# Kernel optimization log

Measured on AMD Instinct MI355X. Metric: run time of the kernel, lower is better.

The kernel has to match this reference:

```python
import jax, jax.numpy as jnp
import numpy as np

B, L, SEQ_D, PAIR_D = 4, 512, 640, 128
C, H, NL = 128, 4, 3
DH = C // H
ED = PAIR_D + 1
KNN_K = 16
E_MAX = 131072
MIN_LOOP, MIN_PROB, HP_THRESH = 4, 0.01, 0.3


def _nussinov_pairs_np(P, min_loop=MIN_LOOP, min_prob=MIN_PROB):
    # Faithful numpy port of the torch.jit Nussinov DP (vectorized over diagonals)
    Ln = P.shape[0]
    S = np.zeros((Ln, Ln), dtype=np.float64)
    lo = np.where(P >= min_prob, np.log(P / (1.0 - P + 1e-9)), 0.0)
    for d in range(min_loop + 1, Ln):
        i = np.arange(Ln - d); j = i + d
        cand = np.maximum(np.maximum(S[i + 1, j], S[i, j - 1]), S[i + 1, j - 1] + lo[i, j])
        cand = np.maximum(cand, 0.0)  # best_bif starts at 0
        if d - min_loop - 1 > 0:
            K = np.arange(1, d - min_loop)
            bif = (S[i[:, None], i[:, None] + K[None, :]] + S[i[:, None] + K[None, :] + 1, j[:, None]]).max(1)
            cand = np.maximum(cand, bif)
        S[i, j] = cand
    pairs = []; stack = [(0, Ln - 1)]; tol = 1e-9
    while stack:
        i, j = stack.pop()
        if i >= j:
            continue
        if abs(S[i, j] - S[i + 1, j]) <= tol:
            stack.append((i + 1, j))
        elif abs(S[i, j] - S[i, j - 1]) <= tol:
            stack.append((i, j - 1))
        elif P[i, j] >= min_prob and abs(S[i, j] - (S[i + 1, j - 1] + lo[i, j])) <= tol:
            pairs.append((i, j)); stack.append((i + 1, j - 1))
        else:
            for k in range(i + 1, j):
                if abs(S[i, j] - (S[i, k] + S[k + 1, j])) <= tol:
                    stack.append((i, k)); stack.append((k + 1, j)); break
    return pairs


def _build_edges_np(coords, bppm):
    # backbone + Nussinov secondary-structure + kNN + high-prob BPPM edges (per sample)
    Ln = coords.shape[0]
    a = np.arange(Ln - 1)
    src = [np.concatenate([a, a + 1])]; dst = [np.concatenate([a + 1, a])]
    ss = _nussinov_pairs_np(bppm)
    pair_set = set((min(s, d), max(s, d)) for s, d in ss)
    if ss:
        s_ = np.array([p[0] for p in ss]); d_ = np.array([p[1] for p in ss])
        src.append(np.concatenate([s_, d_])); dst.append(np.concatenate([d_, s_]))
    dist = np.linalg.norm(coords[:, None, :] - coords[None, :, :], axis=-1)
    np.fill_diagonal(dist, np.inf)
    nn = np.argpartition(dist, KNN_K, axis=1)[:, :KNN_K]
    s_k = np.repeat(np.arange(Ln), KNN_K); d_k = nn.reshape(-1)
    src.append(np.concatenate([s_k, d_k])); dst.append(np.concatenate([d_k, s_k]))
    hp = np.triu(bppm >= HP_THRESH, 1)
    idx = np.arange(Ln - 1); hp[idx, idx + 1] = False
    for (pi, pj) in pair_set:
        hp[pi, pj] = False
    s_h, d_h = np.nonzero(hp)
    src.append(np.concatenate([s_h, d_h])); dst.append(np.concatenate([d_h, s_h]))
    return np.concatenate(src).astype(np.int64), np.concatenate(dst).astype(np.int64)


def _setup_common():
    rng = np.random.default_rng(0)
    seq = rng.standard_normal((B, L, SEQ_D)).astype(np.float32)
    pair = (rng.standard_normal((B, L, L, PAIR_D)) * 0.5).astype(np.float32)
    u = rng.random((B, L, L)) ** 40  # sparse, realistic BPPM (few high-prob pairs)
    bppm = ((u + np.swapaxes(u, 1, 2)) * 0.5).astype(np.float32)
    for b in range(B):
        np.fill_diagonal(bppm[b], 0.0)
    coords = np.cumsum(rng.standard_normal((B, L, 3)) * 2.0, axis=1).astype(np.float32)
    srcs, dsts = [], []
    for b in range(B):
        s, d = _build_edges_np(coords[b], bppm[b].astype(np.float64))
        srcs.append(s + b * L); dsts.append(d + b * L)
    src = np.concatenate(srcs)[:E_MAX]; dst = np.concatenate(dsts)[:E_MAX]
    E = src.shape[0]
    mask = np.zeros(E_MAX, dtype=np.float32); mask[:E] = 1.0
    src_p = np.zeros(E_MAX, dtype=np.int32); src_p[:E] = src
    dst_p = np.zeros(E_MAX, dtype=np.int32); dst_p[:E] = dst

    def w(*shape, scale):
        return (rng.standard_normal(shape) * scale).astype(np.float32)
    params = dict(
        W_in=w(SEQ_D, C, scale=SEQ_D ** -0.5),
        Wq=w(NL, C, C, scale=C ** -0.5), Wk=w(NL, C, C, scale=C ** -0.5),
        Wv=w(NL, C, C, scale=C ** -0.5), Wo=w(NL, C, C, scale=C ** -0.5),
        We=w(NL, ED, C, scale=ED ** -0.5), wd=w(NL, 1, C, scale=0.01),
        wx=w(NL, C, 1, scale=C ** -0.5),
        ln_g=np.ones((NL, C), dtype=np.float32), ln_b=np.zeros((NL, C), dtype=np.float32))
    inp = dict(sequence_rep=seq, pair_rep=pair, bppm=bppm, initial_coords=coords, **params,
               src=src_p, dst=dst_p, edge_mask=mask)
    return {k: jnp.asarray(v) for k, v in inp.items()}


def _seg_softmax(logits, seg, n):
    m = jax.ops.segment_max(logits, seg, num_segments=n)
    m = jnp.where(jnp.isfinite(m), m, 0.0)
    ex = jnp.exp(logits - m[seg])
    den = jax.ops.segment_sum(ex, seg, num_segments=n)
    return ex / (den[seg] + 1e-9)


def _forward(sequence_rep, pair_rep, bppm, initial_coords, W_in, Wq, Wk, Wv, Wo,
             We, wd, wx, ln_g, ln_b, edge_mask, src, dst):
    N = B * L
    h = sequence_rep.reshape(N, SEQ_D) @ W_in          # degree-0 node feats [N,C]
    x = initial_coords.reshape(N, 3)                    # degree-1 node feats [N,3]
    bidx = src // L
    i = src - bidx * L
    j = dst - bidx * L
    # per-edge features: gathered pair embedding + BPPM prob (edge fiber dim = 129)
    e = jnp.concatenate([pair_rep[bidx, i, j], bppm[bidx, i, j][:, None]], axis=-1)
    mask = edge_mask[:, None]
    for l in range(NL):
        rel = x[src] - x[dst]                           # [E,3] equivariant displacement
        d2 = jnp.sum(rel * rel, axis=-1, keepdims=True)  # [E,1] invariant
        q = (h @ Wq[l])[dst].reshape(-1, H, DH)
        k = (h @ Wk[l])[src].reshape(-1, H, DH)
        v = (h @ Wv[l])[src].reshape(-1, H, DH)
        eb = jax.nn.relu(e @ We[l] + d2 * wd[l]).reshape(-1, H, DH)  # edge bias
        logits = jnp.sum(q * (k + eb), axis=-1) / np.sqrt(DH) + (mask - 1.0) * 1e9
        alpha = _seg_softmax(logits, dst, N) * mask     # [E,H] per-destination softmax
        msg = (alpha[..., None] * v).reshape(-1, C)
        agg = jax.ops.segment_sum(msg, dst, num_segments=N)  # [N,C]
        h = h + jax.nn.relu(agg @ Wo[l])
        mu = jnp.mean(h, axis=-1, keepdims=True)
        var = jnp.var(h, axis=-1, keepdims=True)
        h = (h - mu) / jnp.sqrt(var + 1e-5) * ln_g[l] + ln_b[l]
        # equivariant coordinate update (degree-1 channel)
        s = jnp.tanh((k + eb).reshape(-1, C) @ wx[l]) * alpha.mean(-1, keepdims=True) * mask
        dx = jax.ops.segment_sum(s * rel / (jnp.sqrt(d2) + 1.0), dst, num_segments=N)
        x = x + dx
    return x.reshape(B, L, 3)


def setup_inputs() -> dict:
    return _setup_common()


def reference(sequence_rep, pair_rep, bppm, initial_coords, W_in, Wq, Wk, Wv, Wo,
              We, wd, wx, ln_g, ln_b, edge_mask, src, dst):
    return _forward(sequence_rep, pair_rep, bppm, initial_coords, W_in, Wq, Wk, Wv, Wo,
                    We, wd, wx, ln_g, ln_b, edge_mask, src, dst)
```

## Files before the change

kernel.cpp:

```cpp
#include <hip/hip_runtime.h>

#define LSEQ  512
#define NNODE 2048
#define CDIM  128
#define EMAX  131072
#define NLAY  3

typedef float f32x4 __attribute__((ext_vector_type(4)));
typedef unsigned short u16x8 __attribute__((ext_vector_type(8)));

static __device__ __forceinline__ unsigned short f2bf(float x) {
  unsigned u = __float_as_uint(x);
  unsigned r = (u + 0x7fffu + ((u >> 16) & 1u)) >> 16;
  return (unsigned short)r;
}

static __device__ __forceinline__ void mfma16(f32x4& d, f32x4 a, f32x4 b) {
  asm("v_mfma_f32_16x16x32_bf16 %0, %1, %2, %0" : "+v"(d) : "v"(a), "v"(b));
}

__global__ void k_zero(int* __restrict__ p, int n) {
  int i = blockIdx.x * blockDim.x + threadIdx.x;
  if (i < n) p[i] = 0;
}

__global__ void k_count(const int* __restrict__ dst, const float* __restrict__ msk,
                        int* __restrict__ cnt) {
  int e = blockIdx.x * 256 + threadIdx.x;
  if (msk[e] != 0.f) atomicAdd(&cnt[dst[e]], 1);
}

__global__ __launch_bounds__(256) void k_scan(const int* __restrict__ cnt,
                                              int* __restrict__ rowp) {
  __shared__ int lds[256];
  int t = threadIdx.x;
  int loc[8];
  int s = 0;
#pragma unroll
  for (int i = 0; i < 8; ++i) { loc[i] = s; s += cnt[t * 8 + i]; }
  lds[t] = s;
  __syncthreads();
  for (int off = 1; off < 256; off <<= 1) {
    int v = (t >= off) ? lds[t - off] : 0;
    __syncthreads();
    lds[t] += v;
    __syncthreads();
  }
  int base = t ? lds[t - 1] : 0;
#pragma unroll
  for (int i = 0; i < 8; ++i) rowp[t * 8 + i] = base + loc[i];
  if (t == 255) rowp[NNODE] = lds[255];
}

__global__ void k_fill(const int* __restrict__ dst, const float* __restrict__ msk,
                       const int* __restrict__ rowp, int* __restrict__ cur,
                       int* __restrict__ colx) {
  int e = blockIdx.x * 256 + threadIdx.x;
  if (msk[e] != 0.f) {
    int n = dst[e];
    int slot = atomicAdd(&cur[n], 1);
    colx[rowp[n] + slot] = e;
  }
}

__global__ __launch_bounds__(256) void k_hinq(
    const float* __restrict__ seq, const float* __restrict__ Win,
    const float* __restrict__ Wq0, const float* __restrict__ Wk0,
    const float* __restrict__ Wv0, float* __restrict__ h,
    float* __restrict__ hq, float* __restrict__ hk, float* __restrict__ hv) {
  __shared__ float sSeq[4][64];
  __shared__ __align__(16) float sW[64][128];
  __shared__ float sH[4][128];
  const int tid = threadIdx.x;
  const int c = tid & 127, g = tid >> 7;
  const int nb = blockIdx.x * 4;

  float a0 = 0.f, a1 = 0.f;
  for (int kc = 0; kc < 10; ++kc) {
    if (tid < 64) {
      int n = tid >> 4, t4 = tid & 15;
      *(float4*)&sSeq[n][t4 * 4] =
          *(const float4*)&seq[(size_t)(nb + n) * 640 + kc * 64 + t4 * 4];
    }
    const float4* wsrc = (const float4*)(Win + (size_t)kc * 64 * CDIM);
#pragma unroll
    for (int i = 0; i < 8; ++i) ((float4*)sW)[tid + i * 256] = wsrc[tid + i * 256];
    __syncthreads();
#pragma unroll 8
    for (int k = 0; k < 64; ++k) {
      float w = sW[k][c];
      a0 += sSeq[g * 2][k] * w;
      a1 += sSeq[g * 2 + 1][k] * w;
    }
    __syncthreads();
  }
  h[(size_t)(nb + g * 2) * CDIM + c] = a0;
  h[(size_t)(nb + g * 2 + 1) * CDIM + c] = a1;
  sH[g * 2][c] = a0;
  sH[g * 2 + 1][c] = a1;
  __syncthreads();

  for (int ws = 0; ws < 3; ++ws) {
    const float* W = ws == 0 ? Wq0 : (ws == 1 ? Wk0 : Wv0);
    float b0 = 0.f, b1 = 0.f;
    for (int kc = 0; kc < 2; ++kc) {
      const float4* wsrc = (const float4*)(W + (size_t)kc * 64 * CDIM);
#pragma unroll
      for (int i = 0; i < 8; ++i) ((float4*)sW)[tid + i * 256] = wsrc[tid + i * 256];
      __syncthreads();
#pragma unroll 8
      for (int k = 0; k < 64; ++k) {
        float w = sW[k][c];
        b0 += sH[g * 2][kc * 64 + k] * w;
        b1 += sH[g * 2 + 1][kc * 64 + k] * w;
      }
      __syncthreads();
    }
    float* o = ws == 0 ? hq : (ws == 1 ? hk : hv);
    o[(size_t)(nb + g * 2) * CDIM + c] = b0;
    o[(size_t)(nb + g * 2 + 1) * CDIM + c] = b1;
  }
}

__global__ __launch_bounds__(256) void k_ebf(const float* __restrict__ pair,
                                             const int* __restrict__ src,
                                             const int* __restrict__ dst,
                                             unsigned short* __restrict__ Ebf) {
  int tid = threadIdx.x;
  int e = blockIdx.x * 16 + (tid >> 4);
  int t = tid & 15;
  int s_ = src[e], d_ = dst[e];
  int bi = s_ >> 9;
  int j = d_ - (bi << 9);
  const float* rp = pair + ((size_t)s_ * LSEQ + j) * CDIM + t * 8;
  float4 v0 = *(const float4*)rp;
  float4 v1 = *(const float4*)(rp + 4);
  u16x8 ov;
  ov[0] = f2bf(v0.x); ov[1] = f2bf(v0.y); ov[2] = f2bf(v0.z); ov[3] = f2bf(v0.w);
  ov[4] = f2bf(v1.x); ov[5] = f2bf(v1.y); ov[6] = f2bf(v1.z); ov[7] = f2bf(v1.w);
  int byte = e * 256 + ((t * 16) ^ ((e & 7) << 4));
  *(u16x8*)((char*)Ebf + byte) = ov;
}

__global__ __launch_bounds__(256) void k_wprep(const float* __restrict__ We,
                                               unsigned short* __restrict__ WeT) {
  int idx = blockIdx.x * 256 + threadIdx.x;
  int l = idx >> 14;
  int rem = idx & 16383;
  int c = rem >> 7, k = rem & 127;
  WeT[idx] = f2bf(We[(size_t)(l * 129 + k) * 128 + c]);
}

__global__ __launch_bounds__(256) void k_edge_mfma(
    const unsigned short* __restrict__ Ebf, const float* __restrict__ bppm,
    const float* __restrict__ xc, const float* __restrict__ hq,
    const float* __restrict__ hk, const unsigned short* __restrict__ WeTl,
    const float* __restrict__ Wel, const float* __restrict__ wdl,
    const float* __restrict__ wxl, const int* __restrict__ src,
    const int* __restrict__ dst, const float* __restrict__ emask,
    float* __restrict__ logits, float* __restrict__ spre) {
  __shared__ __align__(16) unsigned char sA[16384];
  __shared__ float sPart[4][64];
  __shared__ int sS[64], sD[64];
  __shared__ float sM[64], sBp[64], sD2[64];

  const int tid = threadIdx.x;
  const int w = tid >> 6;
  const int l = tid & 63;
  const int li = l & 15, gi = l >> 4;
  const int base = blockIdx.x * 64;

  f32x4 stg[4];
  const f32x4* gE = (const f32x4*)((const char*)Ebf + (size_t)base * 256);
#pragma unroll
  for (int r = 0; r < 4; ++r) stg[r] = gE[r * 256 + tid];

  f32x4 bf[2][4];
#pragma unroll
  for (int nt = 0; nt < 2; ++nt) {
    int c = w * 32 + nt * 16 + li;
#pragma unroll
    for (int ks = 0; ks < 4; ++ks) {
      int k0 = ks * 32 + gi * 8;
      bf[nt][ks] = *(const f32x4*)((const char*)WeTl + (size_t)(c * 128 + k0) * 2);
    }
  }

  if (tid < 64) {
    int e = base + tid;
    int s_ = src[e], d_ = dst[e];
    sS[tid] = s_; sD[tid] = d_; sM[tid] = emask[e];
    int bi = s_ >> 9;
    int j = d_ - (bi << 9);
    float rx = xc[3 * s_ + 0] - xc[3 * d_ + 0];
    float ry = xc[3 * s_ + 1] - xc[3 * d_ + 1];
    float rz = xc[3 * s_ + 2] - xc[3 * d_ + 2];
    sD2[tid] = rx * rx + ry * ry + rz * rz;
    sBp[tid] = bppm[(size_t)s_ * LSEQ + j];
  }

  f32x4* sA4 = (f32x4*)sA;
#pragma unroll
  for (int r = 0; r < 4; ++r) sA4[r * 256 + tid] = stg[r];
  __syncthreads();

  f32x4 acc[4][2];
#pragma unroll
  for (int m = 0; m < 4; ++m)
#pragma unroll
    for (int nt = 0; nt < 2; ++nt) acc[m][nt] = (f32x4){0.f, 0.f, 0.f, 0.f};

#pragma unroll
  for (int ks = 0; ks < 4; ++ks) {
    f32x4 af[4];
#pragma unroll
    for (int m = 0; m < 4; ++m) {
      int row = m * 16 + li;
      int byte = row * 256 + (((ks * 32 + gi * 8) * 2) ^ ((row & 7) << 4));
      af[m] = *(const f32x4*)(sA + byte);
    }
#pragma unroll
    for (int m = 0; m < 4; ++m) {
      mfma16(acc[m][0], af[m], bf[0][ks]);
      mfma16(acc[m][1], af[m], bf[1][ks]);
    }
  }

  const float rs = 0.17677669529663689f;
  const int c0 = w * 32 + li, c1 = c0 + 16;
  const float w128_0 = Wel[128 * 128 + c0], w128_1 = Wel[128 * 128 + c1];
  const float wd0 = wdl[c0], wd1 = wdl[c1];
  const float wx0 = wxl[c0], wx1 = wxl[c1];

#pragma unroll
  for (int m = 0; m < 4; ++m) {
#pragma unroll
    for (int r = 0; r < 4; ++r) {
      int el = m * 16 + gi * 4 + r;
      float bp = sBp[el], d2 = sD2[el];
      int s_ = sS[el], d_ = sD[el];
      float eb0 = fmaxf(acc[m][0][r] + bp * w128_0 + d2 * wd0, 0.f);
      float eb1 = fmaxf(acc[m][1][r] + bp * w128_1 + d2 * wd1, 0.f);
      float keb0 = hk[s_ * CDIM + c0] + eb0;
      float keb1 = hk[s_ * CDIM + c1] + eb1;
      float lp = hq[d_ * CDIM + c0] * keb0 + hq[d_ * CDIM + c1] * keb1;
      float sp = wx0 * keb0 + wx1 * keb1;
#pragma unroll
      for (int o = 1; o < 16; o <<= 1) {
        lp += __shfl_xor(lp, o);
        sp += __shfl_xor(sp, o);
      }
      if (li == 0) {
        int e = base + el;
        logits[e * 4 + w] = lp * rs + (sM[el] - 1.f) * 1e9f;
        sPart[w][el] = sp;
      }
    }
  }
  __syncthreads();
  if (tid < 64)
    spre[base + tid] =
        tanhf(sPart[0][tid] + sPart[1][tid] + sPart[2][tid] + sPart[3][tid]);
}

__global__ __launch_bounds__(256) void k_aggf(
    const int* __restrict__ rowp, const int* __restrict__ colx,
    const float4* __restrict__ lg4, const float* __restrict__ spre,
    const float* __restrict__ hvin, const int* __restrict__ src,
    const float* __restrict__ xc, float* __restrict__ xn,
    float* __restrict__ agg) {
  const int n = blockIdx.x, tid = threadIdx.x;
  const int w = tid >> 6, lane = tid & 63;
  const int st = rowp[n], deg = rowp[n + 1] - st;

  __shared__ float sA[256][4];
  __shared__ int sSe[256];
  __shared__ float sRed[4][4];
  __shared__ float sAcc[4][128];
  __shared__ float sDx[4][3];

  float m0 = -3e38f, m1 = -3e38f, m2 = -3e38f, m3 = -3e38f;
  for (int i = tid; i < deg; i += 256) {
    float4 lg = lg4[colx[st + i]];
    m0 = fmaxf(m0, lg.x); m1 = fmaxf(m1, lg.y);
    m2 = fmaxf(m2, lg.z); m3 = fmaxf(m3, lg.w);
  }
#pragma unroll
  for (int o = 32; o; o >>= 1) {
    m0 = fmaxf(m0, __shfl_xor(m0, o)); m1 = fmaxf(m1, __shfl_xor(m1, o));
    m2 = fmaxf(m2, __shfl_xor(m2, o)); m3 = fmaxf(m3, __shfl_xor(m3, o));
  }
  if (!lane) { sRed[w][0] = m0; sRed[w][1] = m1; sRed[w][2] = m2; sRed[w][3] = m3; }
  __syncthreads();
  m0 = fmaxf(fmaxf(sRed[0][0], sRed[1][0]), fmaxf(sRed[2][0], sRed[3][0]));
  m1 = fmaxf(fmaxf(sRed[0][1], sRed[1][1]), fmaxf(sRed[2][1], sRed[3][1]));
  m2 = fmaxf(fmaxf(sRed[0][2], sRed[1][2]), fmaxf(sRed[2][2], sRed[3][2]));
  m3 = fmaxf(fmaxf(sRed[0][3], sRed[1][3]), fmaxf(sRed[2][3], sRed[3][3]));
  __syncthreads();

  float dn0 = 0.f, dn1 = 0.f, dn2 = 0.f, dn3 = 0.f;
  for (int i = tid; i < deg; i += 256) {
    float4 lg = lg4[colx[st + i]];
    dn0 += __expf(lg.x - m0); dn1 += __expf(lg.y - m1);
    dn2 += __expf(lg.z - m2); dn3 += __expf(lg.w - m3);
  }
#pragma unroll
  for (int o = 32; o; o >>= 1) {
    dn0 += __shfl_xor(dn0, o); dn1 += __shfl_xor(dn1, o);
    dn2 += __shfl_xor(dn2, o); dn3 += __shfl_xor(dn3, o);
  }
  if (!lane) { sRed[w][0] = dn0; sRed[w][1] = dn1; sRed[w][2] = dn2; sRed[w][3] = dn3; }
  __syncthreads();
  dn0 = sRed[0][0] + sRed[1][0] + sRed[2][0] + sRed[3][0];
  dn1 = sRed[0][1] + sRed[1][1] + sRed[2][1] + sRed[3][1];
  dn2 = sRed[0][2] + sRed[1][2] + sRed[2][2] + sRed[3][2];
  dn3 = sRed[0][3] + sRed[1][3] + sRed[2][3] + sRed[3][3];
  const float r0 = 1.f / (dn0 + 1e-9f), r1 = 1.f / (dn1 + 1e-9f);
  const float r2 = 1.f / (dn2 + 1e-9f), r3 = 1.f / (dn3 + 1e-9f);

  const float xnx = xc[3 * n], xny = xc[3 * n + 1], xnz = xc[3 * n + 2];
  float accA = 0.f, accB = 0.f, dxx = 0.f, dxy = 0.f, dxz = 0.f;
  const int hA = lane >> 5, hB = 2 + (lane >> 5);

  for (int bs = 0; bs < deg; bs += 256) {
    int cnt = min(256, deg - bs);
    __syncthreads();
    if (tid < cnt) {
      int e = colx[st + bs + tid];
      float4 lg = lg4[e];
      float a0 = __expf(lg.x - m0) * r0;
      float a1 = __expf(lg.y - m1) * r1;
      float a2 = __expf(lg.z - m2) * r2;
      float a3 = __expf(lg.w - m3) * r3;
      int se = src[e];
      sA[tid][0] = a0; sA[tid][1] = a1; sA[tid][2] = a2; sA[tid][3] = a3;
      sSe[tid] = se;
      float rx = xc[3 * se + 0] - xnx;
      float ry = xc[3 * se + 1] - xny;
      float rz = xc[3 * se + 2] - xnz;
      float dd = rx * rx + ry * ry + rz * rz;
      float s = spre[e] * (a0 + a1 + a2 + a3) * 0.25f;
      float inv = s / (sqrtf(dd) + 1.f);
      dxx += rx * inv; dxy += ry * inv; dxz += rz * inv;
    }
    __syncthreads();
#pragma unroll 4
    for (int j = w; j < cnt; j += 4) {
      const float* vr = hvin + (size_t)sSe[j] * CDIM;
      accA += sA[j][hA] * vr[lane];
      accB += sA[j][hB] * vr[lane + 64];
    }
  }
  sAcc[w][lane] = accA;
  sAcc[w][64 + lane] = accB;
#pragma unroll
  for (int o = 32; o; o >>= 1) {
    dxx += __shfl_xor(dxx, o);
    dxy += __shfl_xor(dxy, o);
    dxz += __shfl_xor(dxz, o);
  }
  if (!lane) { sDx[w][0] = dxx; sDx[w][1] = dxy; sDx[w][2] = dxz; }
  __syncthreads();
  if (tid == 0) {
    xn[3 * n + 0] = xnx + sDx[0][0] + sDx[1][0] + sDx[2][0] + sDx[3][0];
    xn[3 * n + 1] = xny + sDx[0][1] + sDx[1][1] + sDx[2][1] + sDx[3][1];
    xn[3 * n + 2] = xnz + sDx[0][2] + sDx[1][2] + sDx[2][2] + sDx[3][2];
  }
  if (tid < 128)
    agg[(size_t)n * CDIM + tid] =
        sAcc[0][tid] + sAcc[1][tid] + sAcc[2][tid] + sAcc[3][tid];
}

__global__ __launch_bounds__(256) void k_node(
    const float* __restrict__ agg, const float* __restrict__ hin,
    const float* __restrict__ Wol, const float* __restrict__ gl,
    const float* __restrict__ bl, const float* __restrict__ Wqn,
    const float* __restrict__ Wkn, const float* __restrict__ Wvn,
    float* __restrict__ hout, float* __restrict__ hq,
    float* __restrict__ hk, float* __restrict__ hv) {
  __shared__ float sAg[4][128];
  __shared__ float sHin[4][128];
  __shared__ __align__(16) float sW[64][128];
  __shared__ float sH[4][128];
  __shared__ float sRed[4][2][2];
  const int tid = threadIdx.x;
  const int c = tid & 127, g = tid >> 7;
  const int w = tid >> 6, lane = tid & 63;
  const int nb = blockIdx.x * 4;

  {
    int i = tid & 127, half = tid >> 7;
    int n = i >> 5, t4 = i & 31;
    const float* srcb = half ? hin : agg;
    float* dstb = half ? &sHin[0][0] : &sAg[0][0];
    *(float4*)&dstb[n * 128 + t4 * 4] =
        *(const float4*)&srcb[(size_t)(nb + n) * CDIM + t4 * 4];
  }
  __syncthreads();

  float o0 = 0.f, o1 = 0.f;
  for (int kc = 0; kc < 2; ++kc) {
    const float4* wsrc = (const float4*)(Wol + (size_t)kc * 64 * CDIM);
#pragma unroll
    for (int i = 0; i < 8; ++i) ((float4*)sW)[tid + i * 256] = wsrc[tid + i * 256];
    __syncthreads();
#pragma unroll 8
    for (int k = 0; k < 64; ++k) {
      float wv = sW[k][c];
      o0 += sAg[g * 2][kc * 64 + k] * wv;
      o1 += sAg[g * 2 + 1][kc * 64 + k] * wv;
    }
    __syncthreads();
  }
  float hn0 = sHin[g * 2][c] + fmaxf(o0, 0.f);
  float hn1 = sHin[g * 2 + 1][c] + fmaxf(o1, 0.f);
  float s10 = hn0, s20 = hn0 * hn0, s11 = hn1, s21 = hn1 * hn1;
#pragma unroll
  for (int o = 32; o; o >>= 1) {
    s10 += __shfl_xor(s10, o); s20 += __shfl_xor(s20, o);
    s11 += __shfl_xor(s11, o); s21 += __shfl_xor(s21, o);
  }
  if (!lane) {
    sRed[w][0][0] = s10; sRed[w][0][1] = s20;
    sRed[w][1][0] = s11; sRed[w][1][1] = s21;
  }
  __syncthreads();
  {
    float t10 = sRed[g * 2][0][0] + sRed[g * 2 + 1][0][0];
    float t20 = sRed[g * 2][0][1] + sRed[g * 2 + 1][0][1];
    float t11 = sRed[g * 2][1][0] + sRed[g * 2 + 1][1][0];
    float t21 = sRed[g * 2][1][1] + sRed[g * 2 + 1][1][1];
    float mu0 = t10 * (1.f / 128.f), mu1 = t11 * (1.f / 128.f);
    float v0 = t20 * (1.f / 128.f) - mu0 * mu0;
    float v1 = t21 * (1.f / 128.f) - mu1 * mu1;
    float gg = gl[c], bb = bl[c];
    hn0 = (hn0 - mu0) * rsqrtf(v0 + 1e-5f) * gg + bb;
    hn1 = (hn1 - mu1) * rsqrtf(v1 + 1e-5f) * gg + bb;
  }
  hout[(size_t)(nb + g * 2) * CDIM + c] = hn0;
  hout[(size_t)(nb + g * 2 + 1) * CDIM + c] = hn1;
  sH[g * 2][c] = hn0;
  sH[g * 2 + 1][c] = hn1;
  __syncthreads();

  for (int ws = 0; ws < 3; ++ws) {
    const float* W = ws == 0 ? Wqn : (ws == 1 ? Wkn : Wvn);
    float b0 = 0.f, b1 = 0.f;
    for (int kc = 0; kc < 2; ++kc) {
      const float4* wsrc = (const float4*)(W + (size_t)kc * 64 * CDIM);
#pragma unroll
      for (int i = 0; i < 8; ++i) ((float4*)sW)[tid + i * 256] = wsrc[tid + i * 256];
      __syncthreads();
#pragma unroll 8
      for (int k = 0; k < 64; ++k) {
        float wv = sW[k][c];
        b0 += sH[g * 2][kc * 64 + k] * wv;
        b1 += sH[g * 2 + 1][kc * 64 + k] * wv;
      }
      __syncthreads();
    }
    float* o = ws == 0 ? hq : (ws == 1 ? hk : hv);
    o[(size_t)(nb + g * 2) * CDIM + c] = b0;
    o[(size_t)(nb + g * 2 + 1) * CDIM + c] = b1;
  }
}

extern "C" void kernel_launch(void* const* d_in, const int* in_sizes, int n_in,
                              void* d_out, int out_size, void* d_ws, size_t ws_size,
                              hipStream_t stream) {
  const float* seq    = (const float*)d_in[0];
  const float* pair   = (const float*)d_in[1];
  const float* bppm   = (const float*)d_in[2];
  const float* coords = (const float*)d_in[3];
  const float* Win    = (const float*)d_in[4];
  const float* Wq     = (const float*)d_in[5];
  const float* Wk     = (const float*)d_in[6];
  const float* Wv     = (const float*)d_in[7];
  const float* Wo     = (const float*)d_in[8];
  const float* We     = (const float*)d_in[9];
  const float* wd     = (const float*)d_in[10];
  const float* wx     = (const float*)d_in[11];
  const float* lng    = (const float*)d_in[12];
  const float* lnb    = (const float*)d_in[13];
  const int*   src    = (const int*)d_in[14];
  const int*   dst    = (const int*)d_in[15];
  const float* emask  = (const float*)d_in[16];
  float* out = (float*)d_out;

  size_t off = 0;
  auto take = [&](size_t bytes) {
    void* p = (char*)d_ws + off;
    off += (bytes + 255) & ~(size_t)255;
    return p;
  };
  float* hA     = (float*)take((size_t)NNODE * CDIM * 4);
  float* hB     = (float*)take((size_t)NNODE * CDIM * 4);
  float* hqA    = (float*)take((size_t)NNODE * CDIM * 4);
  float* hkA    = (float*)take((size_t)NNODE * CDIM * 4);
  float* hvA    = (float*)take((size_t)NNODE * CDIM * 4);
  float* hqB    = (float*)take((size_t)NNODE * CDIM * 4);
  float* hkB    = (float*)take((size_t)NNODE * CDIM * 4);
  float* hvB    = (float*)take((size_t)NNODE * CDIM * 4);
  float* logits = (float*)take((size_t)EMAX * 4 * 4);
  float* spre   = (float*)take((size_t)EMAX * 4);
  float* agg    = (float*)take((size_t)NNODE * CDIM * 4);
  float* x0     = (float*)take((size_t)NNODE * 3 * 4);
  float* x1     = (float*)take((size_t)NNODE * 3 * 4);
  int*   cnt    = (int*)take((size_t)NNODE * 2 * 4);
  int*   cur    = cnt + NNODE;
  int*   rowp   = (int*)take((size_t)(NNODE + 1) * 4);
  int*   colx   = (int*)take((size_t)EMAX * 4);
  unsigned short* Ebf = (unsigned short*)take((size_t)EMAX * CDIM * 2);
  unsigned short* WeT = (unsigned short*)take((size_t)NLAY * CDIM * CDIM * 2);

  k_zero<<<(NNODE * 2 + 255) / 256, 256, 0, stream>>>(cnt, NNODE * 2);
  k_count<<<EMAX / 256, 256, 0, stream>>>(dst, emask, cnt);
  k_scan<<<1, 256, 0, stream>>>(cnt, rowp);
  k_fill<<<EMAX / 256, 256, 0, stream>>>(dst, emask, rowp, cur, colx);

  k_ebf<<<EMAX / 16, 256, 0, stream>>>(pair, src, dst, Ebf);
  k_wprep<<<(NLAY * CDIM * CDIM) / 256, 256, 0, stream>>>(We, WeT);
  k_hinq<<<NNODE / 4, 256, 0, stream>>>(seq, Win, Wq, Wk, Wv, hA, hqA, hkA, hvA);

  const float* xc = coords;
  for (int l = 0; l < NLAY; ++l) {
    const float* hqi = (l & 1) ? hqB : hqA;
    const float* hki = (l & 1) ? hkB : hkA;
    const float* hvi = (l & 1) ? hvB : hvA;
    float* hqo = (l & 1) ? hqA : hqB;
    float* hko = (l & 1) ? hkA : hkB;
    float* hvo = (l & 1) ? hvA : hvB;
    const float* hin = (l & 1) ? hB : hA;
    float* hout = (l & 1) ? hA : hB;

    k_edge_mfma<<<EMAX / 64, 256, 0, stream>>>(
        Ebf, bppm, xc, hqi, hki, WeT + (size_t)l * CDIM * CDIM,
        We + (size_t)l * 129 * CDIM, wd + (size_t)l * CDIM,
        wx + (size_t)l * CDIM, src, dst, emask, logits, spre);

    float* xn = (l == NLAY - 1) ? out : (l == 0 ? x0 : x1);
    k_aggf<<<NNODE, 256, 0, stream>>>(rowp, colx, (const float4*)logits, spre,
                                      hvi, src, xc, xn, agg);
    if (l < NLAY - 1)
      k_node<<<NNODE / 4, 256, 0, stream>>>(
          agg, hin, Wo + (size_t)l * CDIM * CDIM, lng + (size_t)l * CDIM,
          lnb + (size_t)l * CDIM, Wq + (size_t)(l + 1) * CDIM * CDIM,
          Wk + (size_t)(l + 1) * CDIM * CDIM, Wv + (size_t)(l + 1) * CDIM * CDIM,
          hout, hqo, hko, hvo);
    xc = xn;
  }
}
```

Baseline: 240.5 us.

## Reorder edges into destination-sorted CSR order and compact masked edges

```diff
diff --git a/kernel.cpp b/kernel.cpp
--- a/kernel.cpp
+++ b/kernel.cpp
@@ -52,14 +52,17 @@
   if (t == 255) rowp[NNODE] = lds[255];
 }
 
-__global__ void k_fill(const int* __restrict__ dst, const float* __restrict__ msk,
-                       const int* __restrict__ rowp, int* __restrict__ cur,
-                       int* __restrict__ colx) {
+__global__ void k_fill(const int* __restrict__ src, const int* __restrict__ dst,
+                       const float* __restrict__ msk, const int* __restrict__ rowp,
+                       int* __restrict__ cur, int* __restrict__ eS,
+                       int* __restrict__ eD) {
   int e = blockIdx.x * 256 + threadIdx.x;
   if (msk[e] != 0.f) {
     int n = dst[e];
     int slot = atomicAdd(&cur[n], 1);
-    colx[rowp[n] + slot] = e;
+    int p = rowp[n] + slot;
+    eS[p] = src[e];
+    eD[p] = n;
   }
 }
 
@@ -123,32 +126,34 @@
 }
 
 __global__ __launch_bounds__(256) void k_ebf(const float* __restrict__ pair,
-                                             const int* __restrict__ src,
-                                             const int* __restrict__ dst,
-                                             unsigned short* __restrict__ Ebf) {
+                                             const int* __restrict__ eS,
+                                             const int* __restrict__ eD,
+                                             unsigned short* __restrict__ Ebf,
+                                             const float* __restrict__ We,
+                                             unsigned short* __restrict__ WeT) {
   int tid = threadIdx.x;
-  int e = blockIdx.x * 16 + (tid >> 4);
+  int pos = blockIdx.x * 16 + (tid >> 4);
   int t = tid & 15;
-  int s_ = src[e], d_ = dst[e];
-  int bi = s_ >> 9;
-  int j = d_ - (bi << 9);
+  int s_ = eS[pos], d_ = eD[pos];
+  int j = d_ - ((s_ >> 9) << 9);
   const float* rp = pair + ((size_t)s_ * LSEQ + j) * CDIM + t * 8;
   float4 v0 = *(const float4*)rp;
   float4 v1 = *(const float4*)(rp + 4);
   u16x8 ov;
   ov[0] = f2bf(v0.x); ov[1] = f2bf(v0.y); ov[2] = f2bf(v0.z); ov[3] = f2bf(v0.w);
   ov[4] = f2bf(v1.x); ov[5] = f2bf(v1.y); ov[6] = f2bf(v1.z); ov[7] = f2bf(v1.w);
-  int byte = e * 256 + ((t * 16) ^ ((e & 7) << 4));
+  int b = pos >> 6, m = (pos >> 4) & 3, li = pos & 15;
+  int ks = t >> 2, gi = t & 3;
+  size_t byte = ((size_t)((b * 16 + ks * 4 + m) * 64 + gi * 16 + li)) * 16;
   *(u16x8*)((char*)Ebf + byte) = ov;
-}
-
-__global__ __launch_bounds__(256) void k_wprep(const float* __restrict__ We,
-                                               unsigned short* __restrict__ WeT) {
-  int idx = blockIdx.x * 256 + threadIdx.x;
-  int l = idx >> 14;
-  int rem = idx & 16383;
-  int c = rem >> 7, k = rem & 127;
-  WeT[idx] = f2bf(We[(size_t)(l * 129 + k) * 128 + c]);
+
+  if (blockIdx.x < 192) {
+    int idx = blockIdx.x * 256 + tid;
+    int l = idx >> 14;
+    int rem = idx & 16383;
+    int c = rem >> 7, k = rem & 127;
+    WeT[idx] = f2bf(We[(size_t)(l * 129 + k) * 128 + c]);
+  }
 }
 
 __global__ __launch_bounds__(256) void k_edge_mfma(
@@ -156,22 +161,22 @@
     const float* __restrict__ xc, const float* __restrict__ hq,
     const float* __restrict__ hk, const unsigned short* __restrict__ WeTl,
     const float* __restrict__ Wel, const float* __restrict__ wdl,
-    const float* __restrict__ wxl, const int* __restrict__ src,
-    const int* __restrict__ dst, const float* __restrict__ emask,
-    float* __restrict__ logits, float* __restrict__ spre) {
+    const float* __restrict__ wxl, const int* __restrict__ eS,
+    const int* __restrict__ eD, float* __restrict__ logits,
+    float* __restrict__ spre) {
   __shared__ __align__(16) unsigned char sA[16384];
+  __shared__ __align__(16) float sEb[64 * 128];
   __shared__ float sPart[4][64];
   __shared__ int sS[64], sD[64];
-  __shared__ float sM[64], sBp[64], sD2[64];
+  __shared__ float sBp[64], sD2[64];
 
   const int tid = threadIdx.x;
-  const int w = tid >> 6;
-  const int l = tid & 63;
+  const int w = tid >> 6, l = tid & 63;
   const int li = l & 15, gi = l >> 4;
-  const int base = blockIdx.x * 64;
+  const int p0 = blockIdx.x * 64;
 
   f32x4 stg[4];
-  const f32x4* gE = (const f32x4*)((const char*)Ebf + (size_t)base * 256);
+  const f32x4* gE = (const f32x4*)((const char*)Ebf + (size_t)p0 * 256);
 #pragma unroll
   for (int r = 0; r < 4; ++r) stg[r] = gE[r * 256 + tid];
 
@@ -187,11 +192,10 @@
   }
 
   if (tid < 64) {
-    int e = base + tid;
-    int s_ = src[e], d_ = dst[e];
-    sS[tid] = s_; sD[tid] = d_; sM[tid] = emask[e];
-    int bi = s_ >> 9;
-    int j = d_ - (bi << 9);
+    int p = p0 + tid;
+    int s_ = eS[p], d_ = eD[p];
+    sS[tid] = s_; sD[tid] = d_;
+    int j = d_ - ((s_ >> 9) << 9);
     float rx = xc[3 * s_ + 0] - xc[3 * d_ + 0];
     float ry = xc[3 * s_ + 1] - xc[3 * d_ + 1];
     float rz = xc[3 * s_ + 2] - xc[3 * d_ + 2];
@@ -214,11 +218,7 @@
   for (int ks = 0; ks < 4; ++ks) {
     f32x4 af[4];
 #pragma unroll
-    for (int m = 0; m < 4; ++m) {
-      int row = m * 16 + li;
-      int byte = row * 256 + (((ks * 32 + gi * 8) * 2) ^ ((row & 7) << 4));
-      af[m] = *(const f32x4*)(sA + byte);
-    }
+    for (int m = 0; m < 4; ++m) af[m] = sA4[(ks * 4 + m) * 64 + l];
 #pragma unroll
     for (int m = 0; m < 4; ++m) {
       mfma16(acc[m][0], af[m], bf[0][ks]);
@@ -226,49 +226,56 @@
     }
   }
 
-  const float rs = 0.17677669529663689f;
   const int c0 = w * 32 + li, c1 = c0 + 16;
   const float w128_0 = Wel[128 * 128 + c0], w128_1 = Wel[128 * 128 + c1];
   const float wd0 = wdl[c0], wd1 = wdl[c1];
-  const float wx0 = wxl[c0], wx1 = wxl[c1];
-
 #pragma unroll
   for (int m = 0; m < 4; ++m) {
 #pragma unroll
     for (int r = 0; r < 4; ++r) {
       int el = m * 16 + gi * 4 + r;
-      float bp = sBp[el], d2 = sD2[el];
-      int s_ = sS[el], d_ = sD[el];
-      float eb0 = fmaxf(acc[m][0][r] + bp * w128_0 + d2 * wd0, 0.f);
-      float eb1 = fmaxf(acc[m][1][r] + bp * w128_1 + d2 * wd1, 0.f);
-      float keb0 = hk[s_ * CDIM + c0] + eb0;
-      float keb1 = hk[s_ * CDIM + c1] + eb1;
-      float lp = hq[d_ * CDIM + c0] * keb0 + hq[d_ * CDIM + c1] * keb1;
-      float sp = wx0 * keb0 + wx1 * keb1;
-#pragma unroll
-      for (int o = 1; o < 16; o <<= 1) {
-        lp += __shfl_xor(lp, o);
-        sp += __shfl_xor(sp, o);
-      }
-      if (li == 0) {
-        int e = base + el;
-        logits[e * 4 + w] = lp * rs + (sM[el] - 1.f) * 1e9f;
-        sPart[w][el] = sp;
-      }
-    }
+      float bp = sBp[el], d2v = sD2[el];
+      float eb0 = fmaxf(acc[m][0][r] + bp * w128_0 + d2v * wd0, 0.f);
+      float eb1 = fmaxf(acc[m][1][r] + bp * w128_1 + d2v * wd1, 0.f);
+      int swz = (el & 7) << 2;
+      sEb[el * 128 + (c0 ^ swz)] = eb0;
+      sEb[el * 128 + (c1 ^ swz)] = eb1;
+    }
+  }
+  __syncthreads();
+
+  {
+    const int s_ = sS[l], d_ = sD[l];
+    const int swz = (l & 7) << 2;
+    const float* hkr = hk + (size_t)s_ * CDIM + w * 32;
+    const float* hqr = hq + (size_t)d_ * CDIM + w * 32;
+    const float* wxr = wxl + w * 32;
+    float lp = 0.f, sp = 0.f;
+#pragma unroll
+    for (int k = 0; k < 8; ++k) {
+      f32x4 ebq = *(const f32x4*)&sEb[l * 128 + ((w * 32 + k * 4) ^ swz)];
+      float4 hkq = *(const float4*)(hkr + k * 4);
+      float4 hqq = *(const float4*)(hqr + k * 4);
+      float4 wxq = *(const float4*)(wxr + k * 4);
+      float keb0 = ebq[0] + hkq.x, keb1 = ebq[1] + hkq.y;
+      float keb2 = ebq[2] + hkq.z, keb3 = ebq[3] + hkq.w;
+      lp += hqq.x * keb0 + hqq.y * keb1 + hqq.z * keb2 + hqq.w * keb3;
+      sp += wxq.x * keb0 + wxq.y * keb1 + wxq.z * keb2 + wxq.w * keb3;
+    }
+    logits[(size_t)(p0 + l) * 4 + w] = lp * 0.17677669529663689f;
+    sPart[w][l] = sp;
   }
   __syncthreads();
   if (tid < 64)
-    spre[base + tid] =
+    spre[p0 + tid] =
         tanhf(sPart[0][tid] + sPart[1][tid] + sPart[2][tid] + sPart[3][tid]);
 }
 
 __global__ __launch_bounds__(256) void k_aggf(
-    const int* __restrict__ rowp, const int* __restrict__ colx,
-    const float4* __restrict__ lg4, const float* __restrict__ spre,
-    const float* __restrict__ hvin, const int* __restrict__ src,
-    const float* __restrict__ xc, float* __restrict__ xn,
-    float* __restrict__ agg) {
+    const int* __restrict__ rowp, const float4* __restrict__ lg4,
+    const float* __restrict__ spre, const float* __restrict__ hvin,
+    const int* __restrict__ eS, const float* __restrict__ xc,
+    float* __restrict__ xn, float* __restrict__ agg) {
   const int n = blockIdx.x, tid = threadIdx.x;
   const int w = tid >> 6, lane = tid & 63;
   const int st = rowp[n], deg = rowp[n + 1] - st;
@@ -276,12 +283,12 @@
   __shared__ float sA[256][4];
   __shared__ int sSe[256];
   __shared__ float sRed[4][4];
-  __shared__ float sAcc[4][128];
+  __shared__ __align__(16) float4 sAccF[8][32];
   __shared__ float sDx[4][3];
 
   float m0 = -3e38f, m1 = -3e38f, m2 = -3e38f, m3 = -3e38f;
   for (int i = tid; i < deg; i += 256) {
-    float4 lg = lg4[colx[st + i]];
+    float4 lg = lg4[st + i];
     m0 = fmaxf(m0, lg.x); m1 = fmaxf(m1, lg.y);
     m2 = fmaxf(m2, lg.z); m3 = fmaxf(m3, lg.w);
   }
@@ -300,7 +307,7 @@
 
   float dn0 = 0.f, dn1 = 0.f, dn2 = 0.f, dn3 = 0.f;
   for (int i = tid; i < deg; i += 256) {
-    float4 lg = lg4[colx[st + i]];
+    float4 lg = lg4[st + i];
     dn0 += __expf(lg.x - m0); dn1 += __expf(lg.y - m1);
     dn2 += __expf(lg.z - m2); dn3 += __expf(lg.w - m3);
   }
@@ -319,40 +326,40 @@
   const float r2 = 1.f / (dn2 + 1e-9f), r3 = 1.f / (dn3 + 1e-9f);
 
   const float xnx = xc[3 * n], xny = xc[3 * n + 1], xnz = xc[3 * n + 2];
-  float accA = 0.f, accB = 0.f, dxx = 0.f, dxy = 0.f, dxz = 0.f;
-  const int hA = lane >> 5, hB = 2 + (lane >> 5);
+  const int ch4 = tid & 31, jg = tid >> 5, hd = ch4 >> 3;
+  float4 acc4 = make_float4(0.f, 0.f, 0.f, 0.f);
+  float dxx = 0.f, dxy = 0.f, dxz = 0.f;
 
   for (int bs = 0; bs < deg; bs += 256) {
     int cnt = min(256, deg - bs);
     __syncthreads();
     if (tid < cnt) {
-      int e = colx[st + bs + tid];
-      float4 lg = lg4[e];
+      int idx = st + bs + tid;
+      float4 lg = lg4[idx];
       float a0 = __expf(lg.x - m0) * r0;
       float a1 = __expf(lg.y - m1) * r1;
       float a2 = __expf(lg.z - m2) * r2;
       float a3 = __expf(lg.w - m3) * r3;
-      int se = src[e];
+      int se = eS[idx];
       sA[tid][0] = a0; sA[tid][1] = a1; sA[tid][2] = a2; sA[tid][3] = a3;
       sSe[tid] = se;
       float rx = xc[3 * se + 0] - xnx;
       float ry = xc[3 * se + 1] - xny;
       float rz = xc[3 * se + 2] - xnz;
       float dd = rx * rx + ry * ry + rz * rz;
-      float s = spre[e] * (a0 + a1 + a2 + a3) * 0.25f;
+      float s = spre[idx] * (a0 + a1 + a2 + a3) * 0.25f;
       float inv = s / (sqrtf(dd) + 1.f);
       dxx += rx * inv; dxy += ry * inv; dxz += rz * inv;
     }
     __syncthreads();
-#pragma unroll 4
-    for (int j = w; j < cnt; j += 4) {
-      const float* vr = hvin + (size_t)sSe[j] * CDIM;
-      accA += sA[j][hA] * vr[lane];
-      accB += sA[j][hB] * vr[lane + 64];
-    }
-  }
-  sAcc[w][lane] = accA;
-  sAcc[w][64 + lane] = accB;
+    for (int j = jg; j < cnt; j += 8) {
+      float a = sA[j][hd];
+      const float4 v = *(const float4*)(hvin + (size_t)sSe[j] * CDIM + ch4 * 4);
+      acc4.x += a * v.x; acc4.y += a * v.y;
+      acc4.z += a * v.z; acc4.w += a * v.w;
+    }
+  }
+  sAccF[jg][ch4] = acc4;
 #pragma unroll
   for (int o = 32; o; o >>= 1) {
     dxx += __shfl_xor(dxx, o);
@@ -366,9 +373,15 @@
     xn[3 * n + 1] = xny + sDx[0][1] + sDx[1][1] + sDx[2][1] + sDx[3][1];
     xn[3 * n + 2] = xnz + sDx[0][2] + sDx[1][2] + sDx[2][2] + sDx[3][2];
   }
-  if (tid < 128)
-    agg[(size_t)n * CDIM + tid] =
-        sAcc[0][tid] + sAcc[1][tid] + sAcc[2][tid] + sAcc[3][tid];
+  if (tid < 32) {
+    float4 s = sAccF[0][tid];
+#pragma unroll
+    for (int g = 1; g < 8; ++g) {
+      float4 v = sAccF[g][tid];
+      s.x += v.x; s.y += v.y; s.z += v.z; s.w += v.w;
+    }
+    *(float4*)&agg[(size_t)n * CDIM + tid * 4] = s;
+  }
 }
 
 __global__ __launch_bounds__(256) void k_node(
@@ -509,17 +522,18 @@
   int*   cnt    = (int*)take((size_t)NNODE * 2 * 4);
   int*   cur    = cnt + NNODE;
   int*   rowp   = (int*)take((size_t)(NNODE + 1) * 4);
-  int*   colx   = (int*)take((size_t)EMAX * 4);
+  int*   eS     = (int*)take((size_t)2 * EMAX * 4);
+  int*   eD     = eS + EMAX;
   unsigned short* Ebf = (unsigned short*)take((size_t)EMAX * CDIM * 2);
   unsigned short* WeT = (unsigned short*)take((size_t)NLAY * CDIM * CDIM * 2);
 
   k_zero<<<(NNODE * 2 + 255) / 256, 256, 0, stream>>>(cnt, NNODE * 2);
+  k_zero<<<(2 * EMAX) / 256, 256, 0, stream>>>(eS, 2 * EMAX);
   k_count<<<EMAX / 256, 256, 0, stream>>>(dst, emask, cnt);
   k_scan<<<1, 256, 0, stream>>>(cnt, rowp);
-  k_fill<<<EMAX / 256, 256, 0, stream>>>(dst, emask, rowp, cur, colx);
-
-  k_ebf<<<EMAX / 16, 256, 0, stream>>>(pair, src, dst, Ebf);
-  k_wprep<<<(NLAY * CDIM * CDIM) / 256, 256, 0, stream>>>(We, WeT);
+  k_fill<<<EMAX / 256, 256, 0, stream>>>(src, dst, emask, rowp, cur, eS, eD);
+
+  k_ebf<<<EMAX / 16, 256, 0, stream>>>(pair, eS, eD, Ebf, We, WeT);
   k_hinq<<<NNODE / 4, 256, 0, stream>>>(seq, Win, Wq, Wk, Wv, hA, hqA, hkA, hvA);
 
   const float* xc = coords;
@@ -536,11 +550,11 @@
     k_edge_mfma<<<EMAX / 64, 256, 0, stream>>>(
         Ebf, bppm, xc, hqi, hki, WeT + (size_t)l * CDIM * CDIM,
         We + (size_t)l * 129 * CDIM, wd + (size_t)l * CDIM,
-        wx + (size_t)l * CDIM, src, dst, emask, logits, spre);
+        wx + (size_t)l * CDIM, eS, eD, logits, spre);
 
     float* xn = (l == NLAY - 1) ? out : (l == 0 ? x0 : x1);
-    k_aggf<<<NNODE, 256, 0, stream>>>(rowp, colx, (const float4*)logits, spre,
-                                      hvi, src, xc, xn, agg);
+    k_aggf<<<NNODE, 256, 0, stream>>>(rowp, (const float4*)logits, spre, hvi,
+                                      eS, xc, xn, agg);
     if (l < NLAY - 1)
       k_node<<<NNODE / 4, 256, 0, stream>>>(
           agg, hin, Wo + (size_t)l * CDIM * CDIM, lng + (size_t)l * CDIM,
```

Measured after the change: 225.5 us. 6.2% less time.
